# Optimization experiments

Hardware: AMD Instinct MI355X
Metric: run time of the kernel (lower is better)

The kernel has to match this reference:

```python
import jax, jax.numpy as jnp
import numpy as np

OMEGA = 32  # recall threshold from init_kwargs


def setup_inputs() -> dict:
    key = jax.random.key(0)
    B, T, F, H = 32, 1024, 256, 256
    stdv = 1.0 / np.sqrt(H).astype(np.float32)
    ks = jax.random.split(key, 10)
    u = lambda k, shape: jax.random.uniform(k, shape, jnp.float32, -stdv, stdv)
    return {
        "x": jax.random.normal(ks[0], (B, T, F), jnp.float32),
        "W": u(ks[1], (F, 4 * H)),
        "U": u(ks[2], (H, 4 * H)),
        "P": u(ks[3], (B, 2 * B)),
        "B_bias": u(ks[4], (4 * H,)),
        "W_r": u(ks[5], (F, 1)),
        "P_r": u(ks[6], (1, B)),
        "U_r": u(ks[7], (H, 1)),
        "W_out": u(ks[8], (H, 1)),
        "b_out": u(ks[9], (1,)),
    }


def reference(x, W, U, P, B_bias, W_r, P_r, U_r, W_out, b_out):
    Bsz, T, F = x.shape
    H = U.shape[0]
    xs = jnp.swapaxes(x, 0, 1)  # [T, B, F]
    h0 = jnp.zeros((Bsz, H), x.dtype)
    c0 = jnp.zeros((Bsz, H), x.dtype)
    Xm0 = jnp.zeros((T, Bsz, F), x.dtype)  # states_array: stored x_t per step
    Hm0 = jnp.zeros((T, Bsz, H), x.dtype)  # states_array: stored h_t per step

    def step(carry, inp):
        h, c, Xm, Hm = carry
        x_t, t = inp  # x_t: [B, F], t: scalar int (== len(states_array) before append)
        # recall gate: sigmoid(P_r @ (x_t @ W_r + h @ U_r)) -> [1,1]
        gate = jax.nn.sigmoid(P_r @ (x_t @ W_r + h @ U_r))[0, 0]
        # best index = round(t * gate); clip to valid range (source would IndexError at t)
        idx = jnp.clip(jnp.round(t.astype(x.dtype) * gate).astype(jnp.int32), 0, jnp.maximum(t - 1, 0))
        use_self = t < OMEGA
        x_rec = jnp.where(use_self, x_t, Xm[idx])
        h_rec = jnp.where(use_self, h, Hm[idx])
        # append current (x_t, h_t) to the memory bank
        Xm = Xm.at[t].set(x_t)
        Hm = Hm.at[t].set(h)
        # x_t_prime = [x_t; x_rec] (2B rows); fold the vstack into a concat of the two affine maps
        a_cur = x_t @ W + h @ U      # [B, 4H]
        a_rec = x_rec @ W + h_rec @ U  # [B, 4H]
        gates = P @ jnp.concatenate([a_cur, a_rec], axis=0) + B_bias  # [B, 4H]
        i_t, f_t, g_t, _o_raw = jnp.split(gates, 4, axis=1)
        i_t = jax.nn.sigmoid(i_t)
        f_t = jax.nn.sigmoid(f_t)
        g_t = jnp.tanh(g_t)
        o_t = i_t  # faithful to source: o_t = sigmoid(i chunk), not the o chunk
        c = f_t * c + i_t * g_t
        h = o_t * jnp.tanh(c)
        return (h, c, Xm, Hm), None

    (h, c, _, _), _ = jax.lax.scan(step, (h0, c0, Xm0, Hm0), (xs, jnp.arange(T)))
    return h @ W_out + b_out  # [B, 1]
```

## Files before the change

### kernel.cpp

```cpp
#include <hip/hip_runtime.h>
#include <cstdint>
#include <cstddef>


#define T_STEPS 1024
#define BSZ 32
#define FDIM 256
#define HDIM 256
#define G3W 384
#define KWG 64
#define HS 4
#define JC 12
#define HPAD 260
#define OMEGA 32
#define HSLICE 8192

static const size_t AXC_BYTES = (size_t)KWG * T_STEPS * G3W * sizeof(float);
static const size_t HB_BYTES  = (size_t)(T_STEPS + 1) * HSLICE * sizeof(float);
static const size_t GX_BYTES  = (size_t)T_STEPS * sizeof(double);

__global__ __launch_bounds__(256) void phaseA(const float* __restrict__ x,
                                              const float* __restrict__ W,
                                              const float* __restrict__ W_r,
                                              const float* __restrict__ P_r,
                                              float* __restrict__ AXc,
                                              double* __restrict__ gx) {
  const int t = blockIdx.x;
  const int tid = threadIdx.x;
  __shared__ __align__(16) float xs[BSZ][HPAD];
  __shared__ double sred[BSZ];

  for (int i = tid; i < BSZ * FDIM / 4; i += 256) {
    const int b = (i * 4) >> 8;
    const int k = (i * 4) & 255;
    *(float4*)&xs[b][k] = *(const float4*)&x[((size_t)b * T_STEPS + t) * FDIM + k];
  }
  __syncthreads();

  for (int pass = 0; pass < 3; ++pass) {
    const int j = pass * 256 + tid;
    float acc[BSZ];
#pragma unroll
    for (int b = 0; b < BSZ; ++b) acc[b] = 0.f;
    for (int k0 = 0; k0 < FDIM; k0 += 4) {
      const float w0 = W[(size_t)(k0 + 0) * 1024 + j];
      const float w1 = W[(size_t)(k0 + 1) * 1024 + j];
      const float w2 = W[(size_t)(k0 + 2) * 1024 + j];
      const float w3 = W[(size_t)(k0 + 3) * 1024 + j];
#pragma unroll
      for (int b = 0; b < BSZ; ++b) {
        const float4 xv = *(const float4*)&xs[b][k0];
        acc[b] = fmaf(xv.x, w0, acc[b]);
        acc[b] = fmaf(xv.y, w1, acc[b]);
        acc[b] = fmaf(xv.z, w2, acc[b]);
        acc[b] = fmaf(xv.w, w3, acc[b]);
      }
    }
    const int wgj = (j >> 2) & 63;
    const int slot = ((j >> 8) << 2) | (j & 3);
    float* dst = AXc + ((size_t)wgj * T_STEPS + t) * G3W + slot;
    for (int b = 0; b < BSZ; ++b) dst[b * 12] = acc[b];
  }

  if (tid < BSZ) {
    double s = 0.0;
    for (int k = 0; k < FDIM; k += 4) {
      const float4 xv = *(const float4*)&xs[tid][k];
      const float4 wv = *(const float4*)&W_r[k];
      s = fma((double)xv.x, (double)wv.x, s);
      s = fma((double)xv.y, (double)wv.y, s);
      s = fma((double)xv.z, (double)wv.z, s);
      s = fma((double)xv.w, (double)wv.w, s);
    }
    sred[tid] = s;
  }
  __syncthreads();
  if (tid == 0) {
    double g = 0.0;
    for (int b = 0; b < BSZ; ++b) g = fma((double)P_r[b], sred[b], g);
    gx[t] = g;
  }
}

__global__ __launch_bounds__(256) void phaseB(const float* __restrict__ U,
                                              const float* __restrict__ P,
                                              const float* __restrict__ B_bias,
                                              const float* __restrict__ P_r,
                                              const float* __restrict__ U_r,
                                              float* __restrict__ AXc,
                                              float* __restrict__ hbank,
                                              const double* __restrict__ gx,
                                              unsigned int* __restrict__ cnt) {
  const int wg = blockIdx.x;
  const int tid = threadIdx.x;
  const int lane = tid & 63;

  __shared__ __align__(16) float ULt[JC][HPAD];
  __shared__ __align__(16) float hL[BSZ][HPAD];
  __shared__ __align__(16) float PL[BSZ][64];
  __shared__ __align__(16) float acs[JC][36];
  __shared__ __align__(16) float ars[JC][36];
  __shared__ __align__(16) float red1[BSZ][JC];
  __shared__ __align__(16) float UrL[FDIM];
  __shared__ float PrL[BSZ];
  __shared__ float biasL[JC];

  for (int i = tid; i < JC * HDIM; i += 256) {
    const int jc = i >> 8, k = i & 255;
    const int col = (jc >> 2) * HDIM + wg * HS + (jc & 3);
    ULt[jc][k] = U[(size_t)k * 1024 + col];
  }
  for (int i = tid; i < BSZ * 64; i += 256) PL[i >> 6][i & 63] = P[i];
  if (tid < FDIM) UrL[tid] = U_r[tid];
  if (tid < BSZ) PrL[tid] = P_r[tid];
  if (tid < JC) biasL[tid] = B_bias[(tid >> 2) * HDIM + wg * HS + (tid & 3)];

  const int u = (tid >= 64) ? (tid - 64) : 0;
  const int khalf = u / 96;
  const int rmap = u % 96;
  const int jcp = rmap % 6, bA = rmap / 6;
  const int jc0 = 2 * jcp, jc1 = jc0 + 1;
  const int bB = bA + 16;
  const int kb = khalf * 128;

  const int ob = tid >> 2, ohc = tid & 3;
  const int grow = tid & 31;
  const int gc0 = (tid >> 5) * 4;

  float* __restrict__ AXwg = AXc + (size_t)wg * T_STEPS * G3W;

  float creg = 0.f;
  __syncthreads();

  for (int t = 0; t < T_STEPS; ++t) {
    float2 xwA = {0.f, 0.f}, xwB = {0.f, 0.f};
    size_t aA = 0, aB = 0;
    if (tid >= 64 && tid < 160) {
      aA = (size_t)t * G3W + bA * JC + jc0;
      aB = (size_t)t * G3W + bB * JC + jc0;
      xwA = *(const float2*)&AXwg[aA];
      xwB = *(const float2*)&AXwg[aB];
    }
    double gxt = 0.0;
    if (tid == 0) gxt = gx[t];

    if (t > 0) {
      if (tid < 64) {
        const unsigned tgt = 8u * (unsigned)t;
        int guard = 0;
        for (;;) {
          unsigned v = tgt;
          if (lane < 8) {
            v = __hip_atomic_load(&cnt[lane * 32], __ATOMIC_RELAXED,
                                  __HIP_MEMORY_SCOPE_AGENT);
          }
          if (__all((int)(v >= tgt))) break;
          if (++guard > (1 << 20)) break;
        }
      }
      __syncthreads();
      asm volatile("" ::: "memory");
    }

    {
      const uint64_t base =
          (uint64_t)(hbank + (size_t)t * HSLICE) + (uint64_t)tid * 16u;
      const uint64_t a0 = base;
      const uint64_t a1 = base + 4096u;
      const uint64_t a2 = base + 8192u;
      const uint64_t a3 = base + 12288u;
      const uint64_t a4 = base + 16384u;
      const uint64_t a5 = base + 20480u;
      const uint64_t a6 = base + 24576u;
      const uint64_t a7 = base + 28672u;
      float4 r0, r1, r2, r3, r4, r5, r6, r7;
      asm volatile(
          "global_load_dwordx4 %0, %8, off sc0 sc1\n\t"
          "global_load_dwordx4 %1, %9, off sc0 sc1\n\t"
          "global_load_dwordx4 %2, %10, off sc0 sc1\n\t"
          "global_load_dwordx4 %3, %11, off sc0 sc1\n\t"
          "global_load_dwordx4 %4, %12, off sc0 sc1\n\t"
          "global_load_dwordx4 %5, %13, off sc0 sc1\n\t"
          "global_load_dwordx4 %6, %14, off sc0 sc1\n\t"
          "global_load_dwordx4 %7, %15, off sc0 sc1\n\t"
          "s_waitcnt vmcnt(0)"
          : "=&v"(r0), "=&v"(r1), "=&v"(r2), "=&v"(r3),
            "=&v"(r4), "=&v"(r5), "=&v"(r6), "=&v"(r7)
          : "v"(a0), "v"(a1), "v"(a2), "v"(a3),
            "v"(a4), "v"(a5), "v"(a6), "v"(a7)
          : "memory");
      *(float4*)&hL[grow][gc0 + 0]   = r0;
      *(float4*)&hL[grow][gc0 + 32]  = r1;
      *(float4*)&hL[grow][gc0 + 64]  = r2;
      *(float4*)&hL[grow][gc0 + 96]  = r3;
      *(float4*)&hL[grow][gc0 + 128] = r4;
      *(float4*)&hL[grow][gc0 + 160] = r5;
      *(float4*)&hL[grow][gc0 + 192] = r6;
      *(float4*)&hL[grow][gc0 + 224] = r7;
    }
    __syncthreads();

    float s00 = 0.f, s01 = 0.f, s10 = 0.f, s11 = 0.f;
    if (tid < 64) {
      if (t >= OMEGA) {
        const int gb = tid & 31, kp = tid >> 5;
        double s = 0.0;
        const int k0 = kp * 128;
        for (int k = k0; k < k0 + 128; k += 4) {
          const float4 hv = *(const float4*)&hL[gb][k];
          const float4 uv = *(const float4*)&UrL[k];
          s = fma((double)hv.x, (double)uv.x, s);
          s = fma((double)hv.y, (double)uv.y, s);
          s = fma((double)hv.z, (double)uv.z, s);
          s = fma((double)hv.w, (double)uv.w, s);
        }
        s += __shfl_xor(s, 32, 64);
        double v = (double)PrL[gb] * s;
        v += __shfl_xor(v, 16, 64);
        v += __shfl_xor(v, 8, 64);
        v += __shfl_xor(v, 4, 64);
        v += __shfl_xor(v, 2, 64);
        v += __shfl_xor(v, 1, 64);
        int idx = 0;
        if (tid == 0) {
          const double g = gxt + v;
          const double gate = 1.0 / (1.0 + exp(-g));
          idx = (int)rint((double)t * gate);
          if (idx > t - 1) idx = t - 1;
          if (idx < 0) idx = 0;
        }
        idx = __shfl(idx, 0, 64);
        const float* __restrict__ src = AXwg + (size_t)idx * G3W;
        float av[6];
#pragma unroll
        for (int j = 0; j < 6; ++j) av[j] = src[lane + j * 64];
#pragma unroll
        for (int j = 0; j < 6; ++j) {
          const int f = lane + j * 64;
          ars[f % JC][f / JC] = av[j];
        }
      }
    } else {
      for (int k = kb; k < kb + 128; k += 4) {
        const float4 u0 = *(const float4*)&ULt[jc0][k];
        const float4 u1 = *(const float4*)&ULt[jc1][k];
        const float4 h0 = *(const float4*)&hL[bA][k];
        const float4 h1 = *(const float4*)&hL[bB][k];
        s00 = fmaf(h0.x, u0.x, s00); s00 = fmaf(h0.y, u0.y, s00);
        s00 = fmaf(h0.z, u0.z, s00); s00 = fmaf(h0.w, u0.w, s00);
        s01 = fmaf(h0.x, u1.x, s01); s01 = fmaf(h0.y, u1.y, s01);
        s01 = fmaf(h0.z, u1.z, s01); s01 = fmaf(h0.w, u1.w, s01);
        s10 = fmaf(h1.x, u0.x, s10); s10 = fmaf(h1.y, u0.y, s10);
        s10 = fmaf(h1.z, u0.z, s10); s10 = fmaf(h1.w, u0.w, s10);
        s11 = fmaf(h1.x, u1.x, s11); s11 = fmaf(h1.y, u1.y, s11);
        s11 = fmaf(h1.z, u1.z, s11); s11 = fmaf(h1.w, u1.w, s11);
      }
      if (khalf == 1) {
        *(float2*)&red1[bA][jc0] = make_float2(s00, s01);
        *(float2*)&red1[bB][jc0] = make_float2(s10, s11);
      }
    }
    __syncthreads();

    if (tid >= 64 && tid < 160) {
      const float2 rA = *(const float2*)&red1[bA][jc0];
      const float2 rB = *(const float2*)&red1[bB][jc0];
      const float v00 = s00 + rA.x + xwA.x;
      const float v01 = s01 + rA.y + xwA.y;
      const float v10 = s10 + rB.x + xwB.x;
      const float v11 = s11 + rB.y + xwB.y;
      *(float2*)&AXwg[aA] = make_float2(v00, v01);
      *(float2*)&AXwg[aB] = make_float2(v10, v11);
      acs[jc0][bA] = v00;  acs[jc1][bA] = v01;
      acs[jc0][bB] = v10;  acs[jc1][bB] = v11;
      if (t < OMEGA) {
        ars[jc0][bA] = v00;  ars[jc1][bA] = v01;
        ars[jc0][bB] = v10;  ars[jc1][bB] = v11;
      }
    }
    __syncthreads();

    if (tid < BSZ * HS) {
      float gi = biasL[ohc];
      float gf = biasL[4 + ohc];
      float gg = biasL[8 + ohc];
#pragma unroll
      for (int b4 = 0; b4 < BSZ; b4 += 4) {
        const float4 pv = *(const float4*)&PL[ob][b4];
        const float4 ai = *(const float4*)&acs[ohc][b4];
        const float4 af = *(const float4*)&acs[4 + ohc][b4];
        const float4 ag = *(const float4*)&acs[8 + ohc][b4];
        gi = fmaf(pv.x, ai.x, gi); gi = fmaf(pv.y, ai.y, gi);
        gi = fmaf(pv.z, ai.z, gi); gi = fmaf(pv.w, ai.w, gi);
        gf = fmaf(pv.x, af.x, gf); gf = fmaf(pv.y, af.y, gf);
        gf = fmaf(pv.z, af.z, gf); gf = fmaf(pv.w, af.w, gf);
        gg = fmaf(pv.x, ag.x, gg); gg = fmaf(pv.y, ag.y, gg);
        gg = fmaf(pv.z, ag.z, gg); gg = fmaf(pv.w, ag.w, gg);
      }
#pragma unroll
      for (int b4 = 0; b4 < BSZ; b4 += 4) {
        const float4 pv = *(const float4*)&PL[ob][BSZ + b4];
        const float4 ai = *(const float4*)&ars[ohc][b4];
        const float4 af = *(const float4*)&ars[4 + ohc][b4];
        const float4 ag = *(const float4*)&ars[8 + ohc][b4];
        gi = fmaf(pv.x, ai.x, gi); gi = fmaf(pv.y, ai.y, gi);
        gi = fmaf(pv.z, ai.z, gi); gi = fmaf(pv.w, ai.w, gi);
        gf = fmaf(pv.x, af.x, gf); gf = fmaf(pv.y, af.y, gf);
        gf = fmaf(pv.z, af.z, gf); gf = fmaf(pv.w, af.w, gf);
        gg = fmaf(pv.x, ag.x, gg); gg = fmaf(pv.y, ag.y, gg);
        gg = fmaf(pv.z, ag.z, gg); gg = fmaf(pv.w, ag.w, gg);
      }
      const float iv = 1.f / (1.f + expf(-gi));
      const float fv = 1.f / (1.f + expf(-gf));
      const float gv = tanhf(gg);
      creg = fmaf(fv, creg, iv * gv);
      const float hv = iv * tanhf(creg);
      const uint64_t daddr =
          (uint64_t)(hbank + (size_t)(t + 1) * HSLICE + (size_t)wg * (BSZ * HS)) +
          (uint64_t)tid * 4u;
      asm volatile(
          "global_store_dword %0, %1, off sc0 sc1\n\t"
          "s_waitcnt vmcnt(0)"
          :: "v"(daddr), "v"(hv)
          : "memory");
    }
    __syncthreads();
    if (tid == 0) {
      __hip_atomic_fetch_add(&cnt[(wg & 7) * 32], 1u, __ATOMIC_RELAXED,
                             __HIP_MEMORY_SCOPE_AGENT);
    }
  }
}

__global__ void outK(const float* __restrict__ hbank, const float* __restrict__ W_out,
                     const float* __restrict__ b_out, float* __restrict__ out) {
  const int b = threadIdx.x;
  if (b < BSZ) {
    const float* h = hbank + (size_t)T_STEPS * HSLICE;
    float s = 0.f;
    for (int wg = 0; wg < KWG; ++wg) {
      const float4 hv = *(const float4*)&h[wg * (BSZ * HS) + b * HS];
      const float4 wv = *(const float4*)&W_out[wg * HS];
      s = fmaf(hv.x, wv.x, s); s = fmaf(hv.y, wv.y, s);
      s = fmaf(hv.z, wv.z, s); s = fmaf(hv.w, wv.w, s);
    }
    out[b] = s + b_out[0];
  }
}

extern "C" void kernel_launch(void* const* d_in, const int* in_sizes, int n_in,
                              void* d_out, int out_size, void* d_ws, size_t ws_size,
                              hipStream_t stream) {
  const float* x      = (const float*)d_in[0];
  const float* W      = (const float*)d_in[1];
  const float* U      = (const float*)d_in[2];
  const float* P      = (const float*)d_in[3];
  const float* B_bias = (const float*)d_in[4];
  const float* W_r    = (const float*)d_in[5];
  const float* P_r    = (const float*)d_in[6];
  const float* U_r    = (const float*)d_in[7];
  const float* W_out  = (const float*)d_in[8];
  const float* b_out  = (const float*)d_in[9];

  char* ws = (char*)d_ws;
  float*    AXc   = (float*)ws;
  float*    hbank = (float*)(ws + AXC_BYTES);
  double*   gx    = (double*)(ws + AXC_BYTES + HB_BYTES);
  unsigned* cnt   = (unsigned*)(ws + AXC_BYTES + HB_BYTES + GX_BYTES);

  hipMemsetAsync(hbank, 0, (size_t)HSLICE * sizeof(float), stream);
  hipMemsetAsync(cnt, 0, 1024, stream);

  phaseA<<<T_STEPS, 256, 0, stream>>>(x, W, W_r, P_r, AXc, gx);
  phaseB<<<KWG, 256, 0, stream>>>(U, P, B_bias, P_r, U_r, AXc, hbank, gx, cnt);
  outK<<<1, 64, 0, stream>>>(hbank, W_out, b_out, (float*)d_out);
}
```

Measured before the change: 5.254 ms.

## Fuse phaseA passes into one k-loop and signal per-wave instead of post-barrier

Result: no change. 5.271 ms (+0.3%).

```diff
diff --git a/kernel.cpp b/kernel.cpp
--- a/kernel.cpp
+++ b/kernel.cpp
@@ -37,29 +37,50 @@
   }
   __syncthreads();
 
-  for (int pass = 0; pass < 3; ++pass) {
-    const int j = pass * 256 + tid;
-    float acc[BSZ];
-#pragma unroll
-    for (int b = 0; b < BSZ; ++b) acc[b] = 0.f;
-    for (int k0 = 0; k0 < FDIM; k0 += 4) {
-      const float w0 = W[(size_t)(k0 + 0) * 1024 + j];
-      const float w1 = W[(size_t)(k0 + 1) * 1024 + j];
-      const float w2 = W[(size_t)(k0 + 2) * 1024 + j];
-      const float w3 = W[(size_t)(k0 + 3) * 1024 + j];
-#pragma unroll
-      for (int b = 0; b < BSZ; ++b) {
-        const float4 xv = *(const float4*)&xs[b][k0];
-        acc[b] = fmaf(xv.x, w0, acc[b]);
-        acc[b] = fmaf(xv.y, w1, acc[b]);
-        acc[b] = fmaf(xv.z, w2, acc[b]);
-        acc[b] = fmaf(xv.w, w3, acc[b]);
-      }
-    }
-    const int wgj = (j >> 2) & 63;
-    const int slot = ((j >> 8) << 2) | (j & 3);
-    float* dst = AXc + ((size_t)wgj * T_STEPS + t) * G3W + slot;
-    for (int b = 0; b < BSZ; ++b) dst[b * 12] = acc[b];
+  float acc0[BSZ], acc1[BSZ], acc2[BSZ];
+#pragma unroll
+  for (int b = 0; b < BSZ; ++b) { acc0[b] = 0.f; acc1[b] = 0.f; acc2[b] = 0.f; }
+
+  for (int k0 = 0; k0 < FDIM; k0 += 4) {
+    const float* Wk0 = &W[(size_t)(k0 + 0) * 1024 + tid];
+    const float* Wk1 = &W[(size_t)(k0 + 1) * 1024 + tid];
+    const float* Wk2 = &W[(size_t)(k0 + 2) * 1024 + tid];
+    const float* Wk3 = &W[(size_t)(k0 + 3) * 1024 + tid];
+    const float wa0 = Wk0[0],   wa1 = Wk1[0],   wa2 = Wk2[0],   wa3 = Wk3[0];
+    const float wb0 = Wk0[256], wb1 = Wk1[256], wb2 = Wk2[256], wb3 = Wk3[256];
+    const float wc0 = Wk0[512], wc1 = Wk1[512], wc2 = Wk2[512], wc3 = Wk3[512];
+#pragma unroll
+    for (int b = 0; b < BSZ; ++b) {
+      const float4 xv = *(const float4*)&xs[b][k0];
+      acc0[b] = fmaf(xv.x, wa0, acc0[b]);
+      acc0[b] = fmaf(xv.y, wa1, acc0[b]);
+      acc0[b] = fmaf(xv.z, wa2, acc0[b]);
+      acc0[b] = fmaf(xv.w, wa3, acc0[b]);
+      acc1[b] = fmaf(xv.x, wb0, acc1[b]);
+      acc1[b] = fmaf(xv.y, wb1, acc1[b]);
+      acc1[b] = fmaf(xv.z, wb2, acc1[b]);
+      acc1[b] = fmaf(xv.w, wb3, acc1[b]);
+      acc2[b] = fmaf(xv.x, wc0, acc2[b]);
+      acc2[b] = fmaf(xv.y, wc1, acc2[b]);
+      acc2[b] = fmaf(xv.z, wc2, acc2[b]);
+      acc2[b] = fmaf(xv.w, wc3, acc2[b]);
+    }
+  }
+
+  {
+    const int j = tid;
+    float* dst = AXc + ((size_t)((j >> 2) & 63) * T_STEPS + t) * G3W + (j & 3);
+    for (int b = 0; b < BSZ; ++b) dst[b * 12] = acc0[b];
+  }
+  {
+    const int j = 256 + tid;
+    float* dst = AXc + ((size_t)((j >> 2) & 63) * T_STEPS + t) * G3W + 4 + (j & 3);
+    for (int b = 0; b < BSZ; ++b) dst[b * 12] = acc1[b];
+  }
+  {
+    const int j = 512 + tid;
+    float* dst = AXc + ((size_t)((j >> 2) & 63) * T_STEPS + t) * G3W + 8 + (j & 3);
+    for (int b = 0; b < BSZ; ++b) dst[b * 12] = acc2[b];
   }
 
   if (tid < BSZ) {
@@ -146,7 +167,7 @@
 
     if (t > 0) {
       if (tid < 64) {
-        const unsigned tgt = 8u * (unsigned)t;
+        const unsigned tgt = 16u * (unsigned)t;
         int guard = 0;
         for (;;) {
           unsigned v = tgt;
@@ -323,11 +344,10 @@
           "s_waitcnt vmcnt(0)"
           :: "v"(daddr), "v"(hv)
           : "memory");
-    }
-    __syncthreads();
-    if (tid == 0) {
-      __hip_atomic_fetch_add(&cnt[(wg & 7) * 32], 1u, __ATOMIC_RELAXED,
-                             __HIP_MEMORY_SCOPE_AGENT);
+      if ((tid & 63) == 0) {
+        __hip_atomic_fetch_add(&cnt[(wg & 7) * 32], 1u, __ATOMIC_RELAXED,
+                               __HIP_MEMORY_SCOPE_AGENT);
+      }
     }
   }
 }
```
